# Optimization experiments

Hardware: AMD Instinct MI355X
Metric: run time of the kernel (lower is better)

## Reference

```python
import jax, jax.numpy as jnp
import numpy as np

B, T, S, D, H = 16, 128, 128, 512, 100

def setup_inputs() -> dict:
    key = jax.random.key(0)
    ks = jax.random.split(key, 10)
    sc = 0.02
    return {
        "input": jax.random.normal(ks[0], (B, T, D), dtype=jnp.float32),
        "memory_bank": jax.random.normal(ks[1], (B, S, D), dtype=jnp.float32),
        "W_in": jax.random.normal(ks[2], (D, D), dtype=jnp.float32) * sc,   # linear_in, no bias
        "W1": jax.random.normal(ks[3], (H, 2 * D), dtype=jnp.float32) * sc,  # linear_1
        "b1": jnp.zeros((H,), dtype=jnp.float32),
        "W2": jax.random.normal(ks[4], (H, H), dtype=jnp.float32) * sc,      # linear_2
        "b2": jnp.zeros((H,), dtype=jnp.float32),
        "w_mean": jax.random.normal(ks[5], (H,), dtype=jnp.float32) * sc,    # mean_out
        "b_mean": jnp.zeros((1,), dtype=jnp.float32),
        "w_var": jax.random.normal(ks[6], (H,), dtype=jnp.float32) * sc,     # var_out
        "b_var": jnp.zeros((1,), dtype=jnp.float32),
        "W_out": jax.random.normal(ks[7], (D, 2 * D), dtype=jnp.float32) * sc,  # linear_out, no bias
    }


def reference(input, memory_bank, W_in, W1, b1, W2, b2, w_mean, b_mean, w_var, b_var, W_out):
    d = input.shape[-1]
    # score(): linear_in(h_t) then bmm with h_s^T -> [B,T,S]
    ht = jnp.einsum('btd,ed->bte', input, W_in)
    align = jnp.einsum('bte,bse->bts', ht, memory_bank)
    # softmax over source dim (no memory_lengths -> no mask)
    align_vectors = jax.nn.softmax(align, axis=-1)
    # get_raw_scores(): fused form of cat([h_t_expand, h_s_expand]) @ W1^T
    W1t, W1s = W1[:, :d], W1[:, d:]
    pt = jnp.einsum('btd,hd->bth', input, W1t)        # [B,T,H]
    ps = jnp.einsum('bsd,hd->bsh', memory_bank, W1s)  # [B,S,H]
    h1 = jax.nn.softplus(pt[:, :, None, :] + ps[:, None, :, :] + b1)  # [B,T,S,H]
    h2 = jax.nn.softplus(jnp.einsum('btsh,gh->btsg', h1, W2) + b2)    # [B,T,S,H]
    h_mean = jax.nn.softplus(jnp.einsum('btsg,g->bts', h2, w_mean) + b_mean[0])
    h_var = jax.nn.softplus(jnp.einsum('btsg,g->bts', h2, w_var) + b_var[0])
    # context + output projection + tanh
    c = jnp.einsum('bts,bsd->btd', align_vectors, memory_bank)
    concat_c = jnp.concatenate([c, input], axis=-1)  # [B,T,2D]
    attn_h = jnp.tanh(jnp.einsum('btf,df->btd', concat_c, W_out))
    # multi-step: transpose to [T,B,*]
    attn_h = jnp.transpose(attn_h, (1, 0, 2))
    align_vectors = jnp.transpose(align_vectors, (1, 0, 2))
    return attn_h, align_vectors, h_mean, h_var
```

## Files before the change

kernel.cpp:

```cpp
#include <hip/hip_runtime.h>
#include <hip/hip_bf16.h>
#include <math.h>

#define Bn 16
#define Tn 128
#define Sn 128
#define Dn 512
#define Hn 100
#define TT2 2

typedef short short8 __attribute__((ext_vector_type(8)));
typedef float f32x4 __attribute__((ext_vector_type(4)));
typedef unsigned short ushort4v __attribute__((ext_vector_type(4)));

__device__ __forceinline__ float softplus_f(float x) {
    return fmaxf(x, 0.0f) + __logf(1.0f + __expf(-fabsf(x)));
}
__device__ __forceinline__ unsigned short f2bf(float f) {
    unsigned u = __float_as_uint(f);
    unsigned r = u + 0x7FFFu + ((u >> 16) & 1u);
    return (unsigned short)(r >> 16);
}
__device__ __forceinline__ float bf2f(unsigned short h) {
    return __uint_as_float(((unsigned)h) << 16);
}
__device__ __forceinline__ unsigned pkrn(float a, float b) {
    __hip_bfloat162 h = __float22bfloat162_rn(float2{a, b});
    return *reinterpret_cast<unsigned*>(&h);
}
struct BfPair { unsigned short h, l; };
__device__ __forceinline__ BfPair split2(float x) {
    BfPair p;
    p.h = f2bf(x);
    p.l = f2bf(x - bf2f(p.h));
    return p;
}

__global__ __launch_bounds__(256)
void conv_trans(const float* __restrict__ input, const float* __restrict__ mem,
                const float* __restrict__ W_in, const float* __restrict__ W1,
                const float* __restrict__ W_out, const float* __restrict__ W2,
                unsigned short* __restrict__ inh, unsigned short* __restrict__ inl,
                unsigned short* __restrict__ memh, unsigned short* __restrict__ meml,
                unsigned short* __restrict__ winh, unsigned short* __restrict__ winl,
                unsigned short* __restrict__ w1b, unsigned short* __restrict__ woutb,
                unsigned short* __restrict__ w2b, unsigned short* __restrict__ concatb,
                unsigned short* __restrict__ memTb)
{
    __shared__ float tile[64][65];
    const int bx = blockIdx.x;
    if (bx >= 2930) {
        const int b2x = bx - 2930;
        const int d0 = (b2x & 7) * 64, s0 = ((b2x >> 3) & 1) * 64, b = b2x >> 4;
        const int tid = threadIdx.x;
        const int r = tid >> 2, cb = (tid & 3) * 16;
        const float* src = mem + ((long)b * Sn + s0 + r) * Dn + d0 + cb;
        #pragma unroll
        for (int j = 0; j < 4; ++j) {
            float4 v = *(const float4*)&src[j * 4];
            tile[r][cb + j * 4 + 0] = v.x;
            tile[r][cb + j * 4 + 1] = v.y;
            tile[r][cb + j * 4 + 2] = v.z;
            tile[r][cb + j * 4 + 3] = v.w;
        }
        __syncthreads();
        unsigned short* dst = memTb + ((long)b * Dn + d0 + r) * Sn + s0 + cb;
        #pragma unroll
        for (int j = 0; j < 4; ++j) {
            ushort4v q;
            q.x = f2bf(tile[cb + j * 4 + 0][r]);
            q.y = f2bf(tile[cb + j * 4 + 1][r]);
            q.z = f2bf(tile[cb + j * 4 + 2][r]);
            q.w = f2bf(tile[cb + j * 4 + 3][r]);
            *(ushort4v*)&dst[j * 4] = q;
        }
        return;
    }
    long gid = (long)bx * 1024 + (long)threadIdx.x * 4;
    if (gid < 1048576) {
        float4 v = *(const float4*)&input[gid];
        BfPair a = split2(v.x), b = split2(v.y), c = split2(v.z), d = split2(v.w);
        ushort4v h = {a.h, b.h, c.h, d.h};
        ushort4v l = {a.l, b.l, c.l, d.l};
        *(ushort4v*)&inh[gid] = h;
        *(ushort4v*)&inl[gid] = l;
        long row = gid >> 9; int col = (int)(gid & 511);
        *(ushort4v*)&concatb[row * 1024 + 512 + col] = h;
    } else if (gid < 2097152) {
        long e = gid - 1048576;
        float4 v = *(const float4*)&mem[e];
        BfPair a = split2(v.x), b = split2(v.y), c = split2(v.z), d = split2(v.w);
        ushort4v h = {a.h, b.h, c.h, d.h};
        ushort4v l = {a.l, b.l, c.l, d.l};
        *(ushort4v*)&memh[e] = h;
        *(ushort4v*)&meml[e] = l;
    } else if (gid < 2359296) {
        long e = gid - 2097152;
        float4 v = *(const float4*)&W_in[e];
        BfPair a = split2(v.x), b = split2(v.y), c = split2(v.z), d = split2(v.w);
        ushort4v h = {a.h, b.h, c.h, d.h};
        ushort4v l = {a.l, b.l, c.l, d.l};
        *(ushort4v*)&winh[e] = h;
        *(ushort4v*)&winl[e] = l;
    } else if (gid < 2461696) {
        long e = gid - 2359296;
        float4 v = *(const float4*)&W1[e];
        ushort4v h = {f2bf(v.x), f2bf(v.y), f2bf(v.z), f2bf(v.w)};
        *(ushort4v*)&w1b[e] = h;
    } else if (gid < 2985984) {
        long e = gid - 2461696;
        float4 v = *(const float4*)&W_out[e];
        ushort4v h = {f2bf(v.x), f2bf(v.y), f2bf(v.z), f2bf(v.w)};
        *(ushort4v*)&woutb[e] = h;
    } else {
        long e = gid - 2985984;
        int n = (int)(e >> 7), k = (int)(e & 127);
        ushort4v h;
        #pragma unroll
        for (int j = 0; j < 4; ++j) {
            int kj = k + j;
            float val = (n < Hn && kj < Hn) ? W2[n * Hn + kj] : 0.0f;
            h[j] = f2bf(val);
        }
        *(ushort4v*)&w2b[n * 128 + k] = h;
    }
}

template<int SPLIT, int EPI, int KSPLIT, int BSEL>
__device__ __forceinline__
void gemm_body(int bx, int by, int bz_in, int upperThresh,
               const unsigned short* __restrict__ Ah, const unsigned short* __restrict__ Al,
               const unsigned short* __restrict__ Bh, const unsigned short* __restrict__ Bl,
               float* __restrict__ C, unsigned short* __restrict__ Cb,
               unsigned short* __restrict__ Cb2, const float* __restrict__ bias,
               int N, int K, int lda, int ldb, int ldc,
               long sA, long sB, long sC, long sKC,
               unsigned short* As_, unsigned short* Bs_)
{
    unsigned short* Asl = As_ + 4096;
    unsigned short* Bsl = Bs_ + 4096;

    const int tid = threadIdx.x;
    const int n0 = bx * 64;
    const long m0 = (long)by * 64;
    int bz = bz_in, kh = 0;
    if (KSPLIT) { bz = bz_in & 15; kh = bz_in >> 4; }
    Ah += (long)bz * sA;
    Bh += (long)bz * sB;
    if (SPLIT) { Al += (long)bz * sA; Bl += (long)bz * sB; }
    const bool upperB = BSEL && (by >= upperThresh);
    if (upperB) Bh += BSEL;

    const int kbeg = KSPLIT ? kh * (K / KSPLIT) : 0;
    const int kend = KSPLIT ? kbeg + (K / KSPLIT) : K;

    const int wid = tid >> 6, lane = tid & 63;
    const int lm = lane & 15, lq = lane >> 4;
    const int wm = wid & 1, wn = wid >> 1;

    const int sr = tid >> 2;
    const int sc = (tid & 3) * 2;
    const bool bok = (n0 + sr) < N;

    f32x4 acc[2][2];
    #pragma unroll
    for (int i = 0; i < 2; ++i)
        #pragma unroll
        for (int j = 0; j < 2; ++j)
            acc[i][j] = (f32x4){0.f, 0.f, 0.f, 0.f};

    short8 pA[2], pB[2], pAl[2], pBl[2];
    const short8 zz = {0, 0, 0, 0, 0, 0, 0, 0};

    #pragma unroll
    for (int i = 0; i < 2; ++i) {
        int c = sc + i;
        pA[i] = *(const short8*)&Ah[(m0 + sr) * lda + kbeg + c * 8];
        if (SPLIT) pAl[i] = *(const short8*)&Al[(m0 + sr) * lda + kbeg + c * 8];
        pB[i] = bok ? *(const short8*)&Bh[(long)(n0 + sr) * ldb + kbeg + c * 8] : zz;
        if (SPLIT) pBl[i] = bok ? *(const short8*)&Bl[(long)(n0 + sr) * ldb + kbeg + c * 8] : zz;
    }

    for (int k0 = kbeg; k0 < kend; k0 += 64) {
        __syncthreads();
        #pragma unroll
        for (int i = 0; i < 2; ++i) {
            int c = sc + i, p = c ^ (sr & 7);
            *(short8*)&As_[sr * 64 + p * 8] = pA[i];
            *(short8*)&Bs_[sr * 64 + p * 8] = pB[i];
            if (SPLIT) {
                *(short8*)&Asl[sr * 64 + p * 8] = pAl[i];
                *(short8*)&Bsl[sr * 64 + p * 8] = pBl[i];
            }
        }
        __syncthreads();
        if (k0 + 64 < kend) {
            const int kn = k0 + 64;
            #pragma unroll
            for (int i = 0; i < 2; ++i) {
                int c = sc + i;
                pA[i] = *(const short8*)&Ah[(m0 + sr) * lda + kn + c * 8];
                if (SPLIT) pAl[i] = *(const short8*)&Al[(m0 + sr) * lda + kn + c * 8];
                pB[i] = bok ? *(const short8*)&Bh[(long)(n0 + sr) * ldb + kn + c * 8] : zz;
                if (SPLIT) pBl[i] = bok ? *(const short8*)&Bl[(long)(n0 + sr) * ldb + kn + c * 8] : zz;
            }
        }
        #pragma unroll
        for (int kst = 0; kst < 2; ++kst) {
            short8 a[2], b[2], a2[2], b2r[2];
            const int pp = (kst * 4 + lq) ^ (lm & 7);
            #pragma unroll
            for (int mt = 0; mt < 2; ++mt) {
                int row = wm * 32 + mt * 16 + lm;
                a[mt] = *(const short8*)&As_[row * 64 + pp * 8];
                if (SPLIT) a2[mt] = *(const short8*)&Asl[row * 64 + pp * 8];
            }
            #pragma unroll
            for (int nt = 0; nt < 2; ++nt) {
                int row = wn * 32 + nt * 16 + lm;
                b[nt] = *(const short8*)&Bs_[row * 64 + pp * 8];
                if (SPLIT) b2r[nt] = *(const short8*)&Bsl[row * 64 + pp * 8];
            }
            #pragma unroll
            for (int mt = 0; mt < 2; ++mt)
                #pragma unroll
                for (int nt = 0; nt < 2; ++nt) {
                    if (SPLIT) {
                        acc[mt][nt] = __builtin_amdgcn_mfma_f32_16x16x32_bf16(
                            a2[mt], b[nt], acc[mt][nt], 0, 0, 0);
                        acc[mt][nt] = __builtin_amdgcn_mfma_f32_16x16x32_bf16(
                            a[mt], b2r[nt], acc[mt][nt], 0, 0, 0);
                    }
                    acc[mt][nt] = __builtin_amdgcn_mfma_f32_16x16x32_bf16(
                        a[mt], b[nt], acc[mt][nt], 0, 0, 0);
                }
        }
    }

    #pragma unroll
    for (int mt = 0; mt < 2; ++mt)
        #pragma unroll
        for (int nt = 0; nt < 2; ++nt)
            #pragma unroll
            for (int r = 0; r < 4; ++r) {
                long m = m0 + wm * 32 + mt * 16 + lq * 4 + r;
                int n = n0 + wn * 32 + nt * 16 + lm;
                float v = acc[mt][nt][r];
                if (EPI == 0) {
                    if (n < N)
                        C[(long)bz * sC + (long)kh * sKC + m * ldc + n] = v;
                } else if (EPI == 1) {
                    unsigned short h = f2bf(v);
                    Cb[m * ldc + n] = h;
                    Cb2[m * ldc + n] = f2bf(v - bf2f(h));
                } else if (EPI == 2) {
                    long bb = m >> 7, tt = m & 127;
                    C[tt * (Bn * Dn) + bb * Dn + n] = tanhf(v);
                } else if (EPI == 3) {
                    Cb[(long)bz * sC + m * ldc + n] = f2bf(v);
                } else {
                    float bb = (!upperB && n < Hn) ? bias[n] : 0.f;
                    C[m * ldc + n] = v + bb;
                }
            }
}

template<int SPLIT, int EPI, int KSPLIT, int BSEL>
__global__ __launch_bounds__(256)
void mfma_gemm3(const unsigned short* __restrict__ Ah, const unsigned short* __restrict__ Al,
                const unsigned short* __restrict__ Bh, const unsigned short* __restrict__ Bl,
                float* __restrict__ C, unsigned short* __restrict__ Cb,
                unsigned short* __restrict__ Cb2, const float* __restrict__ bias,
                int N, int K, int lda, int ldb, int ldc,
                long sA, long sB, long sC, long sKC)
{
    __shared__ __align__(16) unsigned short As_[(SPLIT ? 2 : 1) * 4096];
    __shared__ __align__(16) unsigned short Bs_[(SPLIT ? 2 : 1) * 4096];
    gemm_body<SPLIT, EPI, KSPLIT, BSEL>(blockIdx.x, blockIdx.y, blockIdx.z,
        (int)(gridDim.y >> 1), Ah, Al, Bh, Bl, C, Cb, Cb2, bias,
        N, K, lda, ldb, ldc, sA, sB, sC, sKC, As_, Bs_);
}

__global__ __launch_bounds__(256)
void gemm_ht_ptps(const unsigned short* __restrict__ inh, const unsigned short* __restrict__ inl,
                  const unsigned short* __restrict__ winh, const unsigned short* __restrict__ winl,
                  unsigned short* __restrict__ hth, unsigned short* __restrict__ htl,
                  const unsigned short* __restrict__ w1b, float* __restrict__ ptps,
                  const float* __restrict__ b1)
{
    __shared__ __align__(16) unsigned short As_[8192];
    __shared__ __align__(16) unsigned short Bs_[8192];
    const int id = blockIdx.x;
    if (id < 256) {
        gemm_body<1, 1, 0, 0>(id & 7, id >> 3, 0, 0,
            inh, inl, winh, winl, nullptr, hth, htl, nullptr,
            Dn, Dn, Dn, Dn, Dn, 0L, 0L, 0L, 0L, As_, Bs_);
    } else {
        const int j = id - 256;
        gemm_body<0, 4, 0, 512>(j & 1, j >> 1, 0, 32,
            inh, nullptr, w1b, nullptr, ptps, nullptr, nullptr, b1,
            Hn, Dn, Dn, 2 * Dn, 128, 0L, 0L, 0L, 0L, As_, Bs_);
    }
}

__global__ __launch_bounds__(256)
void mlp_mfma4(const float* __restrict__ ptps,
               const unsigned short* __restrict__ w2b,
               const float* __restrict__ b2,
               const float* __restrict__ w_mean, const float* __restrict__ b_mean,
               const float* __restrict__ w_var, const float* __restrict__ b_var,
               float* __restrict__ mean_out, float* __restrict__ var_out)
{
    __shared__ __align__(16) unsigned short h1s[64 * 128];
    __shared__ __align__(16) unsigned short w2s[112 * 128];
    __shared__ float ptl[TT2][140];
    __shared__ float b2p[112], wmp[112], wvp[112];

    const int tg = blockIdx.x;
    const int b  = blockIdx.y >> 1;
    const int s0 = (blockIdx.y & 1) * 64;
    const int tid = threadIdx.x;

    #pragma unroll
    for (int i0 = 0; i0 < 7; ++i0) {
        int i = tid + i0 * 256;
        int r_ = i >> 4, c_ = i & 15;
        *(short8*)&w2s[r_ * 128 + (c_ ^ (r_ & 7)) * 8] = *(const short8*)&w2b[i * 8];
    }
    {
        int t = tid >> 7, c = tid & 127;
        ptl[t][c + 4 * (c >> 5)] =
            ptps[((long)b * Tn + tg * TT2 + t) * 128 + c];
    }
    if (tid < 112) {
        b2p[tid] = (tid < Hn) ? b2[tid] : 0.f;
        wmp[tid] = (tid < Hn) ? w_mean[tid] : 0.f;
        wvp[tid] = (tid < Hn) ? w_var[tid] : 0.f;
    }

    const int r = tid >> 2, cb = tid & 3;
    float psreg[4][8];
    {
        const float* psrow = ptps + (long)(2048 + b * Sn + s0 + r) * 128;
        #pragma unroll
        for (int i = 0; i < 4; ++i) {
            int col = (cb + 4 * i) * 8;
            *(float4*)&psreg[i][0] = *(const float4*)&psrow[col];
            *(float4*)&psreg[i][4] = *(const float4*)&psrow[col + 4];
        }
    }
    __syncthreads();

    const int wid = tid >> 6, lane = tid & 63;
    const int lm = lane & 15, lq = lane >> 4;
    const float bm = b_mean[0], bv = b_var[0];

    for (int t = 0; t < TT2; ++t) {
        #pragma unroll
        for (int i = 0; i < 4; ++i) {
            const int c = cb + 4 * i;
            const int col = c * 8;
            const int base = col + 4 * (col >> 5);
            float4 pa = *(const float4*)&ptl[t][base];
            float4 pb = *(const float4*)&ptl[t][base + 4];
            float x0 = softplus_f(psreg[i][0] + pa.x);
            float x1 = softplus_f(psreg[i][1] + pa.y);
            float x2 = softplus_f(psreg[i][2] + pa.z);
            float x3 = softplus_f(psreg[i][3] + pa.w);
            float x4 = softplus_f(psreg[i][4] + pb.x);
            float x5 = softplus_f(psreg[i][5] + pb.y);
            float x6 = softplus_f(psreg[i][6] + pb.z);
            float x7 = softplus_f(psreg[i][7] + pb.w);
            uint4 u;
            u.x = pkrn(x0, x1); u.y = pkrn(x2, x3);
            u.z = pkrn(x4, x5); u.w = pkrn(x6, x7);
            *(uint4*)&h1s[r * 128 + (c ^ (r & 7)) * 8] = u;
        }
        __syncthreads();

        f32x4 acc[7];
        #pragma unroll
        for (int j = 0; j < 7; ++j) acc[j] = (f32x4){0.f, 0.f, 0.f, 0.f};
        #pragma unroll
        for (int ks = 0; ks < 4; ++ks) {
            const int p = (ks * 4 + lq) ^ (lm & 7);
            short8 a = *(const short8*)&h1s[(wid * 16 + lm) * 128 + p * 8];
            #pragma unroll
            for (int nt = 0; nt < 7; ++nt) {
                short8 bf = *(const short8*)&w2s[(nt * 16 + lm) * 128 + p * 8];
                acc[nt] = __builtin_amdgcn_mfma_f32_16x16x32_bf16(a, bf, acc[nt], 0, 0, 0);
            }
        }

        float sM[4] = {}, sV[4] = {};
        #pragma unroll
        for (int nt = 0; nt < 7; ++nt) {
            int g = nt * 16 + lm;
            float bg = b2p[g], wm_ = wmp[g], wv_ = wvp[g];
            #pragma unroll
            for (int rr = 0; rr < 4; ++rr) {
                float h2 = softplus_f(acc[nt][rr] + bg);
                sM[rr] = fmaf(h2, wm_, sM[rr]);
                sV[rr] = fmaf(h2, wv_, sV[rr]);
            }
        }
        #pragma unroll
        for (int off = 1; off < 16; off <<= 1)
            #pragma unroll
            for (int rr = 0; rr < 4; ++rr) {
                sM[rr] += __shfl_xor(sM[rr], off);
                sV[rr] += __shfl_xor(sV[rr], off);
            }
        if (lm == 0) {
            const long base = ((long)b * Tn + tg * TT2 + t) * Sn + s0;
            #pragma unroll
            for (int rr = 0; rr < 4; ++rr) {
                int row = wid * 16 + lq * 4 + rr;
                mean_out[base + row] = softplus_f(sM[rr] + bm);
                var_out[base + row]  = softplus_f(sV[rr] + bv);
            }
        }
        __syncthreads();
    }
}

__global__ __launch_bounds__(256)
void softmax_c(const float* __restrict__ algn, long kstride,
               const unsigned short* __restrict__ memTb,
               float* __restrict__ av_out, unsigned short* __restrict__ concatb)
{
    __shared__ __align__(16) unsigned short avs[64 * 128];
    __shared__ __align__(16) unsigned short Bs[64 * 128];

    const int ntb = blockIdx.x, mtb = blockIdx.y, b = blockIdx.z;
    const int tid = threadIdx.x;
    const int r = tid >> 2, q = tid & 3;

    float v[32];
    {
        const float* arow = algn + ((long)b * Tn + mtb * 64 + r) * Sn + q * 32;
        #pragma unroll
        for (int j = 0; j < 8; ++j) {
            float4 a0 = *(const float4*)&arow[j * 4];
            float4 a1 = *(const float4*)&arow[j * 4 + kstride];
            float4 a2 = *(const float4*)&arow[j * 4 + 2 * kstride];
            float4 a3 = *(const float4*)&arow[j * 4 + 3 * kstride];
            v[j * 4 + 0] = a0.x + a1.x + a2.x + a3.x;
            v[j * 4 + 1] = a0.y + a1.y + a2.y + a3.y;
            v[j * 4 + 2] = a0.z + a1.z + a2.z + a3.z;
            v[j * 4 + 3] = a0.w + a1.w + a2.w + a3.w;
        }
    }
    float mx = v[0];
    #pragma unroll
    for (int i = 1; i < 32; ++i) mx = fmaxf(mx, v[i]);
    mx = fmaxf(mx, __shfl_xor(mx, 1));
    mx = fmaxf(mx, __shfl_xor(mx, 2));
    float sum = 0.f;
    #pragma unroll
    for (int i = 0; i < 32; ++i) { v[i] = __expf(v[i] - mx); sum += v[i]; }
    sum += __shfl_xor(sum, 1);
    sum += __shfl_xor(sum, 2);
    const float inv = 1.0f / sum;

    if (ntb == 0) {
        float* dst = av_out + (long)(mtb * 64 + r) * (Bn * Sn) + b * Sn + q * 32;
        #pragma unroll
        for (int j = 0; j < 8; ++j) {
            float4 o = {v[j*4]*inv, v[j*4+1]*inv, v[j*4+2]*inv, v[j*4+3]*inv};
            *(float4*)&dst[j * 4] = o;
        }
    }
    #pragma unroll
    for (int i = 0; i < 4; ++i) {
        int c = q * 4 + i;
        uint4 u;
        u.x = pkrn(v[i*8+0]*inv, v[i*8+1]*inv);
        u.y = pkrn(v[i*8+2]*inv, v[i*8+3]*inv);
        u.z = pkrn(v[i*8+4]*inv, v[i*8+5]*inv);
        u.w = pkrn(v[i*8+6]*inv, v[i*8+7]*inv);
        *(uint4*)&avs[r * 128 + (c ^ (r & 7)) * 8] = u;
    }
    #pragma unroll
    for (int j = 0; j < 4; ++j) {
        int idx = tid * 4 + j;
        int rB = idx >> 4, cB = idx & 15;
        *(short8*)&Bs[rB * 128 + (cB ^ (rB & 7)) * 8] =
            *(const short8*)&memTb[((long)b * Dn + ntb * 64 + rB) * Sn + cB * 8];
    }
    __syncthreads();

    const int wid = tid >> 6, lane = tid & 63;
    const int lm = lane & 15, lq = lane >> 4;
    const int wm = wid & 1, wn = wid >> 1;

    f32x4 acc[2][2];
    #pragma unroll
    for (int i = 0; i < 2; ++i)
        #pragma unroll
        for (int j = 0; j < 2; ++j) acc[i][j] = (f32x4){0.f, 0.f, 0.f, 0.f};

    #pragma unroll
    for (int kk = 0; kk < 4; ++kk) {
        const int p = (kk * 4 + lq) ^ (lm & 7);
        short8 a0 = *(const short8*)&avs[(wm * 32 + lm) * 128 + p * 8];
        short8 a1 = *(const short8*)&avs[(wm * 32 + 16 + lm) * 128 + p * 8];
        short8 b0 = *(const short8*)&Bs[(wn * 32 + lm) * 128 + p * 8];
        short8 b1 = *(const short8*)&Bs[(wn * 32 + 16 + lm) * 128 + p * 8];
        acc[0][0] = __builtin_amdgcn_mfma_f32_16x16x32_bf16(a0, b0, acc[0][0], 0, 0, 0);
        acc[0][1] = __builtin_amdgcn_mfma_f32_16x16x32_bf16(a0, b1, acc[0][1], 0, 0, 0);
        acc[1][0] = __builtin_amdgcn_mfma_f32_16x16x32_bf16(a1, b0, acc[1][0], 0, 0, 0);
        acc[1][1] = __builtin_amdgcn_mfma_f32_16x16x32_bf16(a1, b1, acc[1][1], 0, 0, 0);
    }
    #pragma unroll
    for (int mt = 0; mt < 2; ++mt)
        #pragma unroll
        for (int nt = 0; nt < 2; ++nt)
            #pragma unroll
            for (int rr = 0; rr < 4; ++rr) {
                long mrow = (long)b * Tn + mtb * 64 + wm * 32 + mt * 16 + lq * 4 + rr;
                int n = ntb * 64 + wn * 32 + nt * 16 + lm;
                concatb[mrow * 1024 + n] = f2bf(acc[mt][nt][rr]);
            }
}

extern "C" void kernel_launch(void* const* d_in, const int* in_sizes, int n_in,
                              void* d_out, int out_size, void* d_ws, size_t ws_size,
                              hipStream_t stream)
{
    (void)in_sizes; (void)n_in; (void)out_size; (void)ws_size;

    const float* input  = (const float*)d_in[0];
    const float* mem    = (const float*)d_in[1];
    const float* W_in   = (const float*)d_in[2];
    const float* W1     = (const float*)d_in[3];
    const float* b1     = (const float*)d_in[4];
    const float* W2     = (const float*)d_in[5];
    const float* b2     = (const float*)d_in[6];
    const float* w_mean = (const float*)d_in[7];
    const float* b_mean = (const float*)d_in[8];
    const float* w_var  = (const float*)d_in[9];
    const float* b_var  = (const float*)d_in[10];
    const float* W_out  = (const float*)d_in[11];

    float* out      = (float*)d_out;
    float* attn_out = out;
    float* av_out   = out + (long)Tn * Bn * Dn;
    float* mean_out = av_out + (long)Tn * Bn * Sn;
    float* var_out  = mean_out + (long)Bn * Tn * Sn;

    char* p = (char*)d_ws;
    unsigned short* inh   = (unsigned short*)p; p += 2097152;
    unsigned short* memh  = (unsigned short*)p; p += 2097152;
    unsigned short* inl   = (unsigned short*)p; p += 2097152;
    unsigned short* meml  = (unsigned short*)p; p += 2097152;
    unsigned short* winh  = (unsigned short*)p; p += 524288;
    unsigned short* winl  = (unsigned short*)p; p += 524288;
    unsigned short* w1b   = (unsigned short*)p; p += 204800;
    unsigned short* woutb = (unsigned short*)p; p += 1048576;
    unsigned short* w2b   = (unsigned short*)p; p += 28672;
    unsigned short* memTb = (unsigned short*)p; p += 2097152;
    unsigned short* hth   = (unsigned short*)p; p += 2097152;
    unsigned short* htl   = (unsigned short*)p; p += 2097152;
    float* ptps           = (float*)p;          p += 2097152;
    float* algn           = (float*)p;          p += 4194304;
    unsigned short* concatb = (unsigned short*)p; p += 4194304;

    const long kstride = (long)Bn * Tn * Sn;

    conv_trans<<<dim3(2930 + 256), 256, 0, stream>>>(
        input, mem, W_in, W1, W_out, W2,
        inh, inl, memh, meml, winh, winl, w1b, woutb, w2b, concatb, memTb);

    gemm_ht_ptps<<<dim3(384), 256, 0, stream>>>(
        inh, inl, winh, winl, hth, htl, w1b, ptps, b1);

    mfma_gemm3<1, 0, 4, 0><<<dim3(2, 2, 64), 256, 0, stream>>>(
        hth, htl, memh, meml, algn, nullptr, nullptr, nullptr,
        Sn, Dn, Dn, Dn, Sn, (long)Tn * Dn, (long)Sn * Dn,
        (long)Tn * Sn, kstride);

    mlp_mfma4<<<dim3(Tn / TT2, Bn * 2), 256, 0, stream>>>(
        ptps, w2b, b2, w_mean, b_mean, w_var, b_var, mean_out, var_out);

    softmax_c<<<dim3(8, 2, 16), 256, 0, stream>>>(
        algn, kstride, memTb, av_out, concatb);

    mfma_gemm3<0, 2, 0, 0><<<dim3(8, 32), 256, 0, stream>>>(
        concatb, nullptr, woutb, nullptr, attn_out, nullptr, nullptr, nullptr,
        Dn, 2 * Dn, 2 * Dn, 2 * Dn, Dn, 0L, 0L, 0L, 0L);
}
```

Baseline: 172.5 us.

## Co-schedule MLP blocks with softmax and output GEMM via fused heterogeneous launches

Splits the MLP head across two combined launches: the first runs softmax/context blocks next to half of the MLP blocks, the second runs the output projection GEMM next to the other half. Each MLP block now handles four target rows instead of two, which halves the MLP block count and amortises loading W2 into shared memory. The aim is to fill idle compute units during the small softmax and GEMM stages and to remove launch gaps, at the cost of a shared byte-offset shared-memory layout and more complex block dispatch.

```diff
diff --git a/kernel.cpp b/kernel.cpp
--- a/kernel.cpp
+++ b/kernel.cpp
@@ -7,7 +7,7 @@
 #define Sn 128
 #define Dn 512
 #define Hn 100
-#define TT2 2
+#define TT4 4
 
 typedef short short8 __attribute__((ext_vector_type(8)));
 typedef float f32x4 __attribute__((ext_vector_type(4)));
@@ -303,22 +303,23 @@
     }
 }
 
-__global__ __launch_bounds__(256)
-void mlp_mfma4(const float* __restrict__ ptps,
-               const unsigned short* __restrict__ w2b,
-               const float* __restrict__ b2,
-               const float* __restrict__ w_mean, const float* __restrict__ b_mean,
-               const float* __restrict__ w_var, const float* __restrict__ b_var,
-               float* __restrict__ mean_out, float* __restrict__ var_out)
-{
-    __shared__ __align__(16) unsigned short h1s[64 * 128];
-    __shared__ __align__(16) unsigned short w2s[112 * 128];
-    __shared__ float ptl[TT2][140];
-    __shared__ float b2p[112], wmp[112], wvp[112];
-
-    const int tg = blockIdx.x;
-    const int b  = blockIdx.y >> 1;
-    const int s0 = (blockIdx.y & 1) * 64;
+__device__ __forceinline__
+void mlp_body(int tg, int yid, char* smem,
+              const float* __restrict__ ptps, const unsigned short* __restrict__ w2b,
+              const float* __restrict__ b2,
+              const float* __restrict__ w_mean, const float* __restrict__ b_mean,
+              const float* __restrict__ w_var, const float* __restrict__ b_var,
+              float* __restrict__ mean_out, float* __restrict__ var_out)
+{
+    unsigned short* h1s = (unsigned short*)smem;
+    unsigned short* w2s = (unsigned short*)(smem + 16384);
+    float (*ptl)[140]   = (float(*)[140])(smem + 45056);
+    float* b2p          = (float*)(smem + 47296);
+    float* wmp          = (float*)(smem + 47744);
+    float* wvp          = (float*)(smem + 48192);
+
+    const int b  = yid >> 1;
+    const int s0 = (yid & 1) * 64;
     const int tid = threadIdx.x;
 
     #pragma unroll
@@ -327,10 +328,12 @@
         int r_ = i >> 4, c_ = i & 15;
         *(short8*)&w2s[r_ * 128 + (c_ ^ (r_ & 7)) * 8] = *(const short8*)&w2b[i * 8];
     }
-    {
-        int t = tid >> 7, c = tid & 127;
-        ptl[t][c + 4 * (c >> 5)] =
-            ptps[((long)b * Tn + tg * TT2 + t) * 128 + c];
+    #pragma unroll
+    for (int j = 0; j < 2; ++j) {
+        int i = tid + j * 256;
+        int tt = i >> 7, c = i & 127;
+        ptl[tt][c + 4 * (c >> 5)] =
+            ptps[((long)b * Tn + tg * TT4 + tt) * 128 + c];
     }
     if (tid < 112) {
         b2p[tid] = (tid < Hn) ? b2[tid] : 0.f;
@@ -355,7 +358,7 @@
     const int lm = lane & 15, lq = lane >> 4;
     const float bm = b_mean[0], bv = b_var[0];
 
-    for (int t = 0; t < TT2; ++t) {
+    for (int t = 0; t < TT4; ++t) {
         #pragma unroll
         for (int i = 0; i < 4; ++i) {
             const int c = cb + 4 * i;
@@ -412,7 +415,7 @@
                 sV[rr] += __shfl_xor(sV[rr], off);
             }
         if (lm == 0) {
-            const long base = ((long)b * Tn + tg * TT2 + t) * Sn + s0;
+            const long base = ((long)b * Tn + tg * TT4 + t) * Sn + s0;
             #pragma unroll
             for (int rr = 0; rr < 4; ++rr) {
                 int row = wid * 16 + lq * 4 + rr;
@@ -424,15 +427,15 @@
     }
 }
 
-__global__ __launch_bounds__(256)
-void softmax_c(const float* __restrict__ algn, long kstride,
-               const unsigned short* __restrict__ memTb,
-               float* __restrict__ av_out, unsigned short* __restrict__ concatb)
-{
-    __shared__ __align__(16) unsigned short avs[64 * 128];
-    __shared__ __align__(16) unsigned short Bs[64 * 128];
-
-    const int ntb = blockIdx.x, mtb = blockIdx.y, b = blockIdx.z;
+__device__ __forceinline__
+void softmax_c_body(int ntb, int mtb, int b, char* smem,
+                    const float* __restrict__ algn, long kstride,
+                    const unsigned short* __restrict__ memTb,
+                    float* __restrict__ av_out, unsigned short* __restrict__ concatb)
+{
+    unsigned short* avs = (unsigned short*)smem;
+    unsigned short* Bs  = (unsigned short*)(smem + 16384);
+
     const int tid = threadIdx.x;
     const int r = tid >> 2, q = tid & 3;
 
@@ -522,6 +525,52 @@
                 int n = ntb * 64 + wn * 32 + nt * 16 + lm;
                 concatb[mrow * 1024 + n] = f2bf(acc[mt][nt][rr]);
             }
+}
+
+__global__ __launch_bounds__(256)
+void sm_mlp(const float* __restrict__ algn, long kstride,
+            const unsigned short* __restrict__ memTb,
+            float* __restrict__ av_out, unsigned short* __restrict__ concatb,
+            const float* __restrict__ ptps, const unsigned short* __restrict__ w2b,
+            const float* __restrict__ b2,
+            const float* __restrict__ w_mean, const float* __restrict__ b_mean,
+            const float* __restrict__ w_var, const float* __restrict__ b_var,
+            float* __restrict__ mean_out, float* __restrict__ var_out)
+{
+    __shared__ __align__(16) char smem[48640];
+    const int id = blockIdx.x;
+    if (id < 256) {
+        softmax_c_body(id & 7, (id >> 3) & 1, id >> 4, smem,
+                       algn, kstride, memTb, av_out, concatb);
+    } else {
+        const int mid = id - 256;
+        mlp_body(mid & 31, mid >> 5, smem,
+                 ptps, w2b, b2, w_mean, b_mean, w_var, b_var, mean_out, var_out);
+    }
+}
+
+__global__ __launch_bounds__(256)
+void attn_mlp(const unsigned short* __restrict__ concatb,
+              const unsigned short* __restrict__ woutb,
+              float* __restrict__ attn_out,
+              const float* __restrict__ ptps, const unsigned short* __restrict__ w2b,
+              const float* __restrict__ b2,
+              const float* __restrict__ w_mean, const float* __restrict__ b_mean,
+              const float* __restrict__ w_var, const float* __restrict__ b_var,
+              float* __restrict__ mean_out, float* __restrict__ var_out)
+{
+    __shared__ __align__(16) char smem[48640];
+    const int id = blockIdx.x;
+    if (id < 256) {
+        gemm_body<0, 2, 0, 0>(id & 7, id >> 3, 0, 0,
+            concatb, nullptr, woutb, nullptr, attn_out, nullptr, nullptr, nullptr,
+            Dn, 2 * Dn, 2 * Dn, 2 * Dn, Dn, 0L, 0L, 0L, 0L,
+            (unsigned short*)smem, (unsigned short*)(smem + 8192));
+    } else {
+        const int mid = id - 256;
+        mlp_body(mid & 31, 16 + (mid >> 5), smem,
+                 ptps, w2b, b2, w_mean, b_mean, w_var, b_var, mean_out, var_out);
+    }
 }
 
 extern "C" void kernel_launch(void* const* d_in, const int* in_sizes, int n_in,
@@ -580,13 +629,11 @@
         Sn, Dn, Dn, Dn, Sn, (long)Tn * Dn, (long)Sn * Dn,
         (long)Tn * Sn, kstride);
 
-    mlp_mfma4<<<dim3(Tn / TT2, Bn * 2), 256, 0, stream>>>(
+    sm_mlp<<<dim3(768), 256, 0, stream>>>(
+        algn, kstride, memTb, av_out, concatb,
         ptps, w2b, b2, w_mean, b_mean, w_var, b_var, mean_out, var_out);
 
-    softmax_c<<<dim3(8, 2, 16), 256, 0, stream>>>(
-        algn, kstride, memTb, av_out, concatb);
-
-    mfma_gemm3<0, 2, 0, 0><<<dim3(8, 32), 256, 0, stream>>>(
-        concatb, nullptr, woutb, nullptr, attn_out, nullptr, nullptr, nullptr,
-        Dn, 2 * Dn, 2 * Dn, 2 * Dn, Dn, 0L, 0L, 0L, 0L);
-}
+    attn_mlp<<<dim3(768), 256, 0, stream>>>(
+        concatb, woutb, attn_out,
+        ptps, w2b, b2, w_mean, b_mean, w_var, b_var, mean_out, var_out);
+}
```

New measurement: 170.3 us, median of 2. About the same (-1.3%).
